# Performance work log

Measured on AMD Instinct MI355X. Metric: run time of the kernel, lower is better.

Reference implementation:

```python
import jax, jax.numpy as jnp
import numpy as np

N = 50000        # nodes
E = 800000       # edges (before self-loops)
F_IN = 128       # in_features
HID = 128        # hidden_size
HEADS = 4
NEG_SLOPE = 0.2  # PyG GATConv default


def setup_inputs() -> dict:
    key = jax.random.key(0)
    ks = jax.random.split(key, 16)
    def w(k, shape, fan_in):
        return jax.random.normal(k, shape, dtype=jnp.float32) / np.sqrt(fan_in)
    x = jax.random.normal(ks[0], (N, F_IN), dtype=jnp.float32)
    edge_index = jax.random.randint(ks[1], (2, E), 0, N, dtype=jnp.int64)
    return {
        "x": x,
        "edge_index": edge_index,
        # encoder: HEADS independent GATConv(F_IN -> HID, heads=1)
        "enc_W": w(ks[2], (HEADS, F_IN, HID), F_IN),
        "enc_asrc": w(ks[3], (HEADS, HID), HID),
        "enc_adst": w(ks[4], (HEADS, HID), HID),
        "enc_b": jnp.zeros((HEADS, HID), jnp.float32),
        "enc_lin_W": w(ks[5], (HEADS * HID, HID), HEADS * HID),
        "enc_lin_b": jnp.zeros((HID,), jnp.float32),
        # decoder: HEADS independent GATConv(HID -> F_IN, heads=1)
        "dec_W": w(ks[6], (HEADS, HID, F_IN), HID),
        "dec_asrc": w(ks[7], (HEADS, F_IN), F_IN),
        "dec_adst": w(ks[8], (HEADS, F_IN), F_IN),
        "dec_b": jnp.zeros((HEADS, F_IN), jnp.float32),
        "dec_lin_W": w(ks[9], (HEADS * F_IN, F_IN), HEADS * F_IN),
        "dec_lin_b": jnp.zeros((F_IN,), jnp.float32),
    }


def _gat_head(x, src, dst, W, a_src, a_dst, b, n):
    # PyG GATConv, heads=1: h = xW; e = leaky_relu(a_src.h_src + a_dst.h_dst)
    # alpha = segment-softmax over incoming edges of dst; out = scatter-add + b
    h = x @ W                                   # [n, out]
    e = (h @ a_src)[src] + (h @ a_dst)[dst]     # [Etot]
    e = jax.nn.leaky_relu(e, NEG_SLOPE)
    m = jax.ops.segment_max(e, dst, num_segments=n)
    ew = jnp.exp(e - m[dst])
    denom = jax.ops.segment_sum(ew, dst, num_segments=n)
    alpha = ew / denom[dst]                     # self-loops guarantee denom > 0
    out = jax.ops.segment_sum(alpha[:, None] * h[src], dst, num_segments=n)
    return out + b


def _multihead(x, src, dst, Ws, asrc, adst, bs, lin_W, lin_b, n):
    heads = [_gat_head(x, src, dst, Ws[h], asrc[h], adst[h], bs[h], n)
             for h in range(Ws.shape[0])]
    cat = jnp.concatenate(heads, axis=1)        # [n, heads*out]
    return jax.nn.relu(cat @ lin_W + lin_b)


def reference(x, edge_index, enc_W, enc_asrc, enc_adst, enc_b, enc_lin_W,
              enc_lin_b, dec_W, dec_asrc, dec_adst, dec_b, dec_lin_W,
              dec_lin_b):
    n = x.shape[0]
    loop = jnp.arange(n, dtype=edge_index.dtype)
    src = jnp.concatenate([edge_index[0], loop])  # add self-loops (PyG default)
    dst = jnp.concatenate([edge_index[1], loop])
    enc = _multihead(x, src, dst, enc_W, enc_asrc, enc_adst, enc_b,
                     enc_lin_W, enc_lin_b, n)
    dec = _multihead(enc, src, dst, dec_W, dec_asrc, dec_adst, dec_b,
                     dec_lin_W, dec_lin_b, n)
    return dec
```

## Files before the change

kernel.cpp:

```cpp
#include <hip/hip_runtime.h>
#include <hip/hip_fp16.h>
#include <cstdint>
#include <cstddef>


#define FDIM   128
#define HEADS  4
#define HCAT   512

typedef unsigned short u16;
typedef __attribute__((ext_vector_type(4))) float f32x4;
typedef __attribute__((ext_vector_type(8))) _Float16 f16x8;

__device__ __forceinline__ u16 f2h_bits(float f) {
    _Float16 h = (_Float16)f;
    return *(u16*)&h;
}

__global__ void k_detect_zero(const void* ei, int E, int N, int* flag, int* deg) {
    int i = blockIdx.x * blockDim.x + threadIdx.x;
    if (i < N) deg[i] = 0;
    if (i == 0) {
        const long long* p = (const long long*)ei;
        int bad = 0;
        int n = E < 64 ? E : 64;
        for (int k = 0; k < n; ++k) {
            long long v = p[k];
            if (v < 0 || v >= (long long)N) bad = 1;
        }
        *flag = bad;
    }
}

__device__ __forceinline__ int edge_at(const void* ei, int is32, long long pos) {
    return is32 ? ((const int*)ei)[pos] : (int)(((const long long*)ei)[pos]);
}

__global__ void k_count(const void* ei, const int* flag, int E, int N, int* deg) {
    int e = blockIdx.x * blockDim.x + threadIdx.x;
    int Etot = E + N;
    if (e >= Etot) return;
    int is32 = *flag;
    int dst = (e < E) ? edge_at(ei, is32, (long long)E + e) : (e - E);
    atomicAdd(&deg[dst], 1);
}

#define SCAN_BLOCKS 256
#define SCAN_TPB    256

__global__ __launch_bounds__(SCAN_TPB) void k_scan1(const int* __restrict__ deg,
                                                    int* __restrict__ bsum, int N) {
    __shared__ int sdata[SCAN_TPB];
    int b = blockIdx.x;
    int chunk = (N + SCAN_BLOCKS - 1) / SCAN_BLOCKS;
    int start = b * chunk;
    int end = start + chunk;
    if (start > N) start = N;
    if (end > N) end = N;
    int s = 0;
    for (int i = start + threadIdx.x; i < end; i += SCAN_TPB) s += deg[i];
    sdata[threadIdx.x] = s;
    __syncthreads();
    for (int o = SCAN_TPB / 2; o; o >>= 1) {
        if (threadIdx.x < o) sdata[threadIdx.x] += sdata[threadIdx.x + o];
        __syncthreads();
    }
    if (threadIdx.x == 0) bsum[b] = sdata[0];
}

__global__ __launch_bounds__(SCAN_BLOCKS) void k_scan2(const int* __restrict__ bsum,
                                                       int* __restrict__ bbase,
                                                       int* __restrict__ off_last) {
    __shared__ int sdata[SCAN_BLOCKS];
    int t = threadIdx.x;
    sdata[t] = bsum[t];
    __syncthreads();
    for (int o = 1; o < SCAN_BLOCKS; o <<= 1) {
        int v = (t >= o) ? sdata[t - o] : 0;
        __syncthreads();
        sdata[t] += v;
        __syncthreads();
    }
    bbase[t] = (t == 0) ? 0 : sdata[t - 1];
    if (t == SCAN_BLOCKS - 1) *off_last = sdata[t];
}

__global__ __launch_bounds__(SCAN_TPB) void k_scan3(const int* __restrict__ deg,
                                                    const int* __restrict__ bbase,
                                                    int* __restrict__ off,
                                                    int* __restrict__ cur, int N) {
    __shared__ int sdata[SCAN_TPB];
    int b = blockIdx.x;
    int chunk = (N + SCAN_BLOCKS - 1) / SCAN_BLOCKS;
    int start = b * chunk;
    int end = start + chunk;
    if (start > N) start = N;
    if (end > N) end = N;
    int base = bbase[b];
    for (int i0 = start; i0 < end; i0 += SCAN_TPB) {
        int i = i0 + threadIdx.x;
        int v = (i < end) ? deg[i] : 0;
        sdata[threadIdx.x] = v;
        __syncthreads();
        for (int o = 1; o < SCAN_TPB; o <<= 1) {
            int u = (threadIdx.x >= o) ? sdata[threadIdx.x - o] : 0;
            __syncthreads();
            sdata[threadIdx.x] += u;
            __syncthreads();
        }
        if (i < end) {
            int excl = base + sdata[threadIdx.x] - v;
            off[i] = excl;
            cur[i] = excl;
        }
        base += sdata[SCAN_TPB - 1];
        __syncthreads();
    }
}

__global__ void k_fill(const void* ei, const int* flag, int E, int N, int* cur, int* csr) {
    int e = blockIdx.x * blockDim.x + threadIdx.x;
    int Etot = E + N;
    if (e >= Etot) return;
    int is32 = *flag;
    int src, dst;
    if (e < E) {
        src = edge_at(ei, is32, e);
        dst = edge_at(ei, is32, (long long)E + e);
    } else {
        src = e - E;
        dst = e - E;
    }
    int pos = atomicAdd(&cur[dst], 1);
    csr[pos] = src;
}

__global__ void k_prep(const float* __restrict__ x, u16* __restrict__ xh, int Nf,
                       const float* __restrict__ encW, u16* __restrict__ eh,
                       const float* __restrict__ linW, u16* __restrict__ lh,
                       const float* __restrict__ decW, u16* __restrict__ dh,
                       const float* __restrict__ dlW, u16* __restrict__ dh2) {
    int i = blockIdx.x * blockDim.x + threadIdx.x;
    if (i < Nf) {
        xh[i] = f2h_bits(x[i]);
        return;
    }
    int j = i - Nf;
    const int WSZ = HEADS * FDIM * FDIM;
    const float* W;
    u16* hi;
    int K;
    if (j < WSZ)            { W = encW; hi = eh;  K = FDIM; }
    else if (j < 2 * WSZ)   { W = linW; hi = lh;  K = HCAT; j -= WSZ; }
    else if (j < 3 * WSZ)   { W = decW; hi = dh;  K = FDIM; j -= 2 * WSZ; }
    else if (j < 4 * WSZ)   { W = dlW;  hi = dh2; K = HCAT; j -= 3 * WSZ; }
    else return;
    int blk = j / (K * 128);
    int rem = j - blk * K * 128;
    int k = rem >> 7, col = rem & 127;
    hi[(size_t)blk * 128 * K + (size_t)col * K + k] = f2h_bits(W[j]);
}

template <int MODE>
__global__ __launch_bounds__(256) void k_gemm_f16(
    const u16* __restrict__ A, int lda,
    const u16* __restrict__ Bt,
    const float* __restrict__ bias,
    const float* __restrict__ asrc, const float* __restrict__ adst,
    float* __restrict__ C, u16* __restrict__ Cb1,
    float* __restrict__ ssrc, float* __restrict__ sdst,
    int ldc, int M, int K)
{
    __shared__ alignas(16) char smem[16384];
    __shared__ float sred[512];
    const int ASH = 0, BHI = 8192;
    int tid = threadIdx.x;
    int bm0 = blockIdx.x * 128;
    int yb = blockIdx.y;

    int wid = tid >> 6, lane = tid & 63;
    int wr = wid >> 1, wc = wid & 1;
    int fr = lane & 15, g = lane >> 4;

    f32x4 acc[4][4] = {};

    int arow = tid >> 1, ahalf = tid & 1;
    bool ain = (bm0 + arow) < M;
    const u16* aptr = A + (size_t)(bm0 + arow) * lda + ahalf * 16;
    int bcol = tid & 127, bhalf = tid >> 7;
    const u16* bph = Bt + (size_t)yb * 128 * K + (size_t)bcol * K + bhalf * 16;

    int abase = arow * 64 + ahalf * 32;
    int asw = (arow & 7) << 4;
    int bbase = bcol * 64 + bhalf * 32;
    int bsw = (bcol & 7) << 4;

    uint4 va0, va1, vb0, vb1;
    if (ain) { va0 = *(const uint4*)(aptr); va1 = *(const uint4*)(aptr + 8); }
    else { va0 = make_uint4(0, 0, 0, 0); va1 = make_uint4(0, 0, 0, 0); }
    vb0 = *(const uint4*)(bph);
    vb1 = *(const uint4*)(bph + 8);

    for (int k0 = 0; k0 < K; k0 += 32) {
        *(uint4*)(smem + ASH + ((abase +  0) ^ asw)) = va0;
        *(uint4*)(smem + ASH + ((abase + 16) ^ asw)) = va1;
        *(uint4*)(smem + BHI + ((bbase +  0) ^ bsw)) = vb0;
        *(uint4*)(smem + BHI + ((bbase + 16) ^ bsw)) = vb1;

        __syncthreads();

        if (k0 + 32 < K) {
            int kn = k0 + 32;
            if (ain) { va0 = *(const uint4*)(aptr + kn); va1 = *(const uint4*)(aptr + kn + 8); }
            else { va0 = make_uint4(0, 0, 0, 0); va1 = make_uint4(0, 0, 0, 0); }
            vb0 = *(const uint4*)(bph + kn);
            vb1 = *(const uint4*)(bph + kn + 8);
        }

        f16x8 af[4], bh[4];
#pragma unroll
        for (int mi = 0; mi < 4; ++mi) {
            int r = wr * 64 + mi * 16 + fr;
            int off = (r * 64 + g * 16) ^ ((r & 7) << 4);
            af[mi] = *(f16x8*)(smem + ASH + off);
        }
#pragma unroll
        for (int nj = 0; nj < 4; ++nj) {
            int c = wc * 64 + nj * 16 + fr;
            int off = (c * 64 + g * 16) ^ ((c & 7) << 4);
            bh[nj] = *(f16x8*)(smem + BHI + off);
        }

#pragma unroll
        for (int mi = 0; mi < 4; ++mi)
#pragma unroll
            for (int nj = 0; nj < 4; ++nj)
                acc[mi][nj] = __builtin_amdgcn_mfma_f32_16x16x32_f16(af[mi], bh[nj], acc[mi][nj], 0, 0, 0);
        __syncthreads();
    }

#pragma unroll
    for (int mi = 0; mi < 4; ++mi) {
#pragma unroll
        for (int q = 0; q < 4; ++q) {
            int r = bm0 + wr * 64 + mi * 16 + g * 4 + q;
            if (r >= M) continue;
#pragma unroll
            for (int nj = 0; nj < 4; ++nj) {
                int c = wc * 64 + nj * 16 + fr;
                float v = acc[mi][nj][q];
                if (MODE == 0) {
                    Cb1[(size_t)r * ldc + yb * 128 + c] = f2h_bits(v);
                } else if (MODE == 1) {
                    v += bias[c];
                    v = fmaxf(v, 0.f);
                    Cb1[(size_t)r * ldc + c] = f2h_bits(v);
                } else {
                    v += bias[c];
                    v = fmaxf(v, 0.f);
                    C[(size_t)r * ldc + c] = v;
                }
            }
        }
    }

    if (MODE == 0) {
        float asv[4], adv[4];
        const float* app = asrc + yb * FDIM;
        const float* dpp = adst + yb * FDIM;
#pragma unroll
        for (int nj = 0; nj < 4; ++nj) {
            int c = wc * 64 + nj * 16 + fr;
            asv[nj] = app[c];
            adv[nj] = dpp[c];
        }
#pragma unroll
        for (int mi = 0; mi < 4; ++mi) {
#pragma unroll
            for (int q = 0; q < 4; ++q) {
                float ps = 0.f, pd = 0.f;
#pragma unroll
                for (int nj = 0; nj < 4; ++nj) {
                    ps += acc[mi][nj][q] * asv[nj];
                    pd += acc[mi][nj][q] * adv[nj];
                }
#pragma unroll
                for (int o = 1; o < 16; o <<= 1) {
                    ps += __shfl_xor(ps, o);
                    pd += __shfl_xor(pd, o);
                }
                if (fr == 0) {
                    int row128 = wr * 64 + mi * 16 + g * 4 + q;
                    sred[(row128 * 2 + wc) * 2 + 0] = ps;
                    sred[(row128 * 2 + wc) * 2 + 1] = pd;
                }
            }
        }
        __syncthreads();
        {
            int rg = tid >> 1;
            int which = tid & 1;
            int r = bm0 + rg;
            if (r < M) {
                float v = sred[(rg * 2 + 0) * 2 + which] + sred[(rg * 2 + 1) * 2 + which];
                float* dstp = which ? sdst : ssrc;
                dstp[(size_t)yb * M + r] = v;
            }
        }
    }
}

__global__ __launch_bounds__(64) void k_aggregate(
    const u16* __restrict__ Hb, const int* __restrict__ off,
    const int* __restrict__ csr, const float* __restrict__ ssrc,
    const float* __restrict__ sdst, const float* __restrict__ bvec,
    u16* __restrict__ Gh, int N) {
    int n = blockIdx.x;
    int lane = threadIdx.x;
    int o0 = __builtin_amdgcn_readfirstlane(off[n]);
    int o1 = __builtin_amdgcn_readfirstlane(off[n + 1]);
    int h = lane >> 4;
    int col0 = lane * 8;
    float sdh = sdst[(size_t)h * N + n];
    const float* ssrc_h = ssrc + (size_t)h * N;
    float denom = 0.f;
    float acc[8] = {0.f, 0.f, 0.f, 0.f, 0.f, 0.f, 0.f, 0.f};

    auto body = [&](float ew, uint4 hv) {
        const __half2* hp = (const __half2*)&hv;
#pragma unroll
        for (int j = 0; j < 4; ++j) {
            float2 f = __half22float2(hp[j]);
            acc[2 * j]     += ew * f.x;
            acc[2 * j + 1] += ew * f.y;
        }
    };

    int i = o0;
    for (; i + 4 <= o1; i += 4) {
        int s0 = csr[i + 0], s1 = csr[i + 1], s2 = csr[i + 2], s3 = csr[i + 3];
        uint4 v0 = *(const uint4*)&Hb[(size_t)s0 * HCAT + col0];
        uint4 v1 = *(const uint4*)&Hb[(size_t)s1 * HCAT + col0];
        uint4 v2 = *(const uint4*)&Hb[(size_t)s2 * HCAT + col0];
        uint4 v3 = *(const uint4*)&Hb[(size_t)s3 * HCAT + col0];
        float e0 = ssrc_h[s0] + sdh, e1 = ssrc_h[s1] + sdh;
        float e2 = ssrc_h[s2] + sdh, e3 = ssrc_h[s3] + sdh;
        e0 = e0 >= 0.f ? e0 : 0.2f * e0;
        e1 = e1 >= 0.f ? e1 : 0.2f * e1;
        e2 = e2 >= 0.f ? e2 : 0.2f * e2;
        e3 = e3 >= 0.f ? e3 : 0.2f * e3;
        float w0 = __expf(e0), w1 = __expf(e1), w2 = __expf(e2), w3 = __expf(e3);
        denom += (w0 + w1) + (w2 + w3);
        body(w0, v0);
        body(w1, v1);
        body(w2, v2);
        body(w3, v3);
    }
    for (; i < o1; ++i) {
        int s = csr[i];
        uint4 v = *(const uint4*)&Hb[(size_t)s * HCAT + col0];
        float e = ssrc_h[s] + sdh;
        e = e >= 0.f ? e : 0.2f * e;
        float ew = __expf(e);
        denom += ew;
        body(ew, v);
    }

    float inv = 1.f / denom;
    u16 hs[8];
#pragma unroll
    for (int k = 0; k < 8; ++k) {
        int col = col0 + k;
        float v = acc[k] * inv + bvec[h * FDIM + (col & 127)];
        hs[k] = f2h_bits(v);
    }
    *(uint4*)&Gh[(size_t)n * HCAT + col0] = *(uint4*)hs;
}

extern "C" void kernel_launch(void* const* d_in, const int* in_sizes, int n_in,
                              void* d_out, int out_size, void* d_ws, size_t ws_size,
                              hipStream_t stream) {
    const float* x = (const float*)d_in[0];
    const void* ei = d_in[1];
    const float* encW = (const float*)d_in[2];
    const float* enc_asrc = (const float*)d_in[3];
    const float* enc_adst = (const float*)d_in[4];
    const float* enc_b = (const float*)d_in[5];
    const float* enc_linW = (const float*)d_in[6];
    const float* enc_linb = (const float*)d_in[7];
    const float* decW = (const float*)d_in[8];
    const float* dec_asrc = (const float*)d_in[9];
    const float* dec_adst = (const float*)d_in[10];
    const float* dec_b = (const float*)d_in[11];
    const float* dec_linW = (const float*)d_in[12];
    const float* dec_linb = (const float*)d_in[13];

    int N = in_sizes[0] / FDIM;
    int E = in_sizes[1] / 2;
    int Etot = E + N;

    char* w = (char*)d_ws;
    size_t o = 0;
    auto alloc = [&](size_t bytes) -> char* {
        char* p = w + o;
        o += (bytes + 255) & ~(size_t)255;
        return p;
    };
    int* flag = (int*)alloc(4);
    int* deg = (int*)alloc((size_t)N * 4);
    int* off = (int*)alloc((size_t)(N + 1) * 4);
    int* cur = (int*)alloc((size_t)N * 4);
    int* csr = (int*)alloc((size_t)Etot * 4);
    int* bsum = (int*)alloc(SCAN_BLOCKS * 4);
    int* bbase = (int*)alloc(SCAN_BLOCKS * 4);
    float* ssrc = (float*)alloc((size_t)HEADS * N * 4);
    float* sdst = (float*)alloc((size_t)HEADS * N * 4);
    u16* Gh = (u16*)alloc((size_t)N * HCAT * 2);
    u16* Hb = (u16*)alloc((size_t)N * HCAT * 2);
    u16* xh = (u16*)alloc((size_t)N * FDIM * 2);
    u16* X2h = (u16*)alloc((size_t)N * FDIM * 2);
    u16* encWt_h = (u16*)alloc((size_t)HEADS * FDIM * FDIM * 2);
    u16* linWt_h = (u16*)alloc((size_t)HCAT * FDIM * 2);
    u16* decWt_h = (u16*)alloc((size_t)HEADS * FDIM * FDIM * 2);
    u16* dlinWt_h = (u16*)alloc((size_t)HCAT * FDIM * 2);
    (void)ws_size;

    k_detect_zero<<<(N + 255) / 256, 256, 0, stream>>>(ei, E, N, flag, deg);
    k_count<<<(Etot + 255) / 256, 256, 0, stream>>>(ei, flag, E, N, deg);
    k_scan1<<<SCAN_BLOCKS, SCAN_TPB, 0, stream>>>(deg, bsum, N);
    k_scan2<<<1, SCAN_BLOCKS, 0, stream>>>(bsum, bbase, off + N);
    k_scan3<<<SCAN_BLOCKS, SCAN_TPB, 0, stream>>>(deg, bbase, off, cur, N);
    k_fill<<<(Etot + 255) / 256, 256, 0, stream>>>(ei, flag, E, N, cur, csr);

    int Nf = N * FDIM;
    int prep_total = Nf + 4 * HEADS * FDIM * FDIM;
    k_prep<<<(prep_total + 255) / 256, 256, 0, stream>>>(
        x, xh, Nf,
        encW, encWt_h,
        enc_linW, linWt_h,
        decW, decWt_h,
        dec_linW, dlinWt_h);

    int mblocks = (N + 127) / 128;

    k_gemm_f16<0><<<dim3(mblocks, 4), 256, 0, stream>>>(
        xh, FDIM, encWt_h, nullptr, enc_asrc, enc_adst,
        nullptr, Hb, ssrc, sdst, HCAT, N, FDIM);
    k_aggregate<<<N, 64, 0, stream>>>(Hb, off, csr, ssrc, sdst, enc_b, Gh, N);
    k_gemm_f16<1><<<dim3(mblocks, 1), 256, 0, stream>>>(
        Gh, HCAT, linWt_h, enc_linb, nullptr, nullptr,
        nullptr, X2h, nullptr, nullptr, FDIM, N, HCAT);

    k_gemm_f16<0><<<dim3(mblocks, 4), 256, 0, stream>>>(
        X2h, FDIM, decWt_h, nullptr, dec_asrc, dec_adst,
        nullptr, Hb, ssrc, sdst, HCAT, N, FDIM);
    k_aggregate<<<N, 64, 0, stream>>>(Hb, off, csr, ssrc, sdst, dec_b, Gh, N);
    k_gemm_f16<2><<<dim3(mblocks, 1), 256, 0, stream>>>(
        Gh, HCAT, dlinWt_h, dec_linb, nullptr, nullptr,
        (float*)d_out, nullptr, nullptr, nullptr, FDIM, N, HCAT);
}
```

Measured before the change: 491.1 us.

## Load full K=128 tiles once in head GEMM and pack four nodes per aggregate block

Adds a dedicated head-projection GEMM that loads the whole 128-deep A and B tiles into 64KB of LDS in one pass, removing the per-k-step double sync loop. The linear GEMMs keep the pipelined loop but drop the head-score epilogue. The aggregate kernel now runs four nodes per 256-thread block instead of one node per 64-thread block, cutting the block count and per-block launch overhead. The larger LDS use may lower GEMM occupancy.

```diff
diff --git a/kernel.cpp b/kernel.cpp
--- a/kernel.cpp
+++ b/kernel.cpp
@@ -161,19 +161,17 @@
     hi[(size_t)blk * 128 * K + (size_t)col * K + k] = f2h_bits(W[j]);
 }
 
-template <int MODE>
-__global__ __launch_bounds__(256) void k_gemm_f16(
-    const u16* __restrict__ A, int lda,
+__global__ __launch_bounds__(256) void k_headgemm(
+    const u16* __restrict__ A,
     const u16* __restrict__ Bt,
-    const float* __restrict__ bias,
     const float* __restrict__ asrc, const float* __restrict__ adst,
-    float* __restrict__ C, u16* __restrict__ Cb1,
+    u16* __restrict__ Hb,
     float* __restrict__ ssrc, float* __restrict__ sdst,
-    int ldc, int M, int K)
+    int M)
 {
-    __shared__ alignas(16) char smem[16384];
+    __shared__ alignas(16) char smem[65536];
     __shared__ float sred[512];
-    const int ASH = 0, BHI = 8192;
+    const int ASH = 0, BSH = 32768;
     int tid = threadIdx.x;
     int bm0 = blockIdx.x * 128;
     int yb = blockIdx.y;
@@ -182,61 +180,42 @@
     int wr = wid >> 1, wc = wid & 1;
     int fr = lane & 15, g = lane >> 4;
 
+    {
+        int row = tid >> 1, half = tid & 1;
+        bool ain = (bm0 + row) < M;
+        const u16* ap = A + (size_t)(bm0 + row) * FDIM + half * 64;
+        const u16* bp = Bt + ((size_t)yb * 128 + row) * FDIM + half * 64;
+        int sw = (row & 7) << 4;
+#pragma unroll
+        for (int j = 0; j < 8; ++j) {
+            uint4 va = ain ? *(const uint4*)(ap + j * 8) : make_uint4(0, 0, 0, 0);
+            uint4 vb = *(const uint4*)(bp + j * 8);
+            *(uint4*)(smem + ASH + ((row * 256 + half * 128 + j * 16) ^ sw)) = va;
+            *(uint4*)(smem + BSH + ((row * 256 + half * 128 + j * 16) ^ sw)) = vb;
+        }
+    }
+    __syncthreads();
+
     f32x4 acc[4][4] = {};
-
-    int arow = tid >> 1, ahalf = tid & 1;
-    bool ain = (bm0 + arow) < M;
-    const u16* aptr = A + (size_t)(bm0 + arow) * lda + ahalf * 16;
-    int bcol = tid & 127, bhalf = tid >> 7;
-    const u16* bph = Bt + (size_t)yb * 128 * K + (size_t)bcol * K + bhalf * 16;
-
-    int abase = arow * 64 + ahalf * 32;
-    int asw = (arow & 7) << 4;
-    int bbase = bcol * 64 + bhalf * 32;
-    int bsw = (bcol & 7) << 4;
-
-    uint4 va0, va1, vb0, vb1;
-    if (ain) { va0 = *(const uint4*)(aptr); va1 = *(const uint4*)(aptr + 8); }
-    else { va0 = make_uint4(0, 0, 0, 0); va1 = make_uint4(0, 0, 0, 0); }
-    vb0 = *(const uint4*)(bph);
-    vb1 = *(const uint4*)(bph + 8);
-
-    for (int k0 = 0; k0 < K; k0 += 32) {
-        *(uint4*)(smem + ASH + ((abase +  0) ^ asw)) = va0;
-        *(uint4*)(smem + ASH + ((abase + 16) ^ asw)) = va1;
-        *(uint4*)(smem + BHI + ((bbase +  0) ^ bsw)) = vb0;
-        *(uint4*)(smem + BHI + ((bbase + 16) ^ bsw)) = vb1;
-
-        __syncthreads();
-
-        if (k0 + 32 < K) {
-            int kn = k0 + 32;
-            if (ain) { va0 = *(const uint4*)(aptr + kn); va1 = *(const uint4*)(aptr + kn + 8); }
-            else { va0 = make_uint4(0, 0, 0, 0); va1 = make_uint4(0, 0, 0, 0); }
-            vb0 = *(const uint4*)(bph + kn);
-            vb1 = *(const uint4*)(bph + kn + 8);
-        }
-
+#pragma unroll
+    for (int ks = 0; ks < 4; ++ks) {
+        int kb = ks * 64 + g * 16;
         f16x8 af[4], bh[4];
 #pragma unroll
         for (int mi = 0; mi < 4; ++mi) {
             int r = wr * 64 + mi * 16 + fr;
-            int off = (r * 64 + g * 16) ^ ((r & 7) << 4);
-            af[mi] = *(f16x8*)(smem + ASH + off);
+            af[mi] = *(f16x8*)(smem + ASH + ((r * 256 + kb) ^ ((r & 7) << 4)));
         }
 #pragma unroll
         for (int nj = 0; nj < 4; ++nj) {
             int c = wc * 64 + nj * 16 + fr;
-            int off = (c * 64 + g * 16) ^ ((c & 7) << 4);
-            bh[nj] = *(f16x8*)(smem + BHI + off);
-        }
-
+            bh[nj] = *(f16x8*)(smem + BSH + ((c * 256 + kb) ^ ((c & 7) << 4)));
+        }
 #pragma unroll
         for (int mi = 0; mi < 4; ++mi)
 #pragma unroll
             for (int nj = 0; nj < 4; ++nj)
                 acc[mi][nj] = __builtin_amdgcn_mfma_f32_16x16x32_f16(af[mi], bh[nj], acc[mi][nj], 0, 0, 0);
-        __syncthreads();
     }
 
 #pragma unroll
@@ -248,23 +227,12 @@
 #pragma unroll
             for (int nj = 0; nj < 4; ++nj) {
                 int c = wc * 64 + nj * 16 + fr;
-                float v = acc[mi][nj][q];
-                if (MODE == 0) {
-                    Cb1[(size_t)r * ldc + yb * 128 + c] = f2h_bits(v);
-                } else if (MODE == 1) {
-                    v += bias[c];
-                    v = fmaxf(v, 0.f);
-                    Cb1[(size_t)r * ldc + c] = f2h_bits(v);
-                } else {
-                    v += bias[c];
-                    v = fmaxf(v, 0.f);
-                    C[(size_t)r * ldc + c] = v;
-                }
+                Hb[(size_t)r * HCAT + yb * 128 + c] = f2h_bits(acc[mi][nj][q]);
             }
         }
     }
 
-    if (MODE == 0) {
+    {
         float asv[4], adv[4];
         const float* app = asrc + yb * FDIM;
         const float* dpp = adst + yb * FDIM;
@@ -310,13 +278,110 @@
     }
 }
 
-__global__ __launch_bounds__(64) void k_aggregate(
+template <int MODE>
+__global__ __launch_bounds__(256) void k_gemm_f16(
+    const u16* __restrict__ A, int lda,
+    const u16* __restrict__ Bt,
+    const float* __restrict__ bias,
+    float* __restrict__ C, u16* __restrict__ Cb1,
+    int ldc, int M, int K)
+{
+    __shared__ alignas(16) char smem[16384];
+    const int ASH = 0, BHI = 8192;
+    int tid = threadIdx.x;
+    int bm0 = blockIdx.x * 128;
+
+    int wid = tid >> 6, lane = tid & 63;
+    int wr = wid >> 1, wc = wid & 1;
+    int fr = lane & 15, g = lane >> 4;
+
+    f32x4 acc[4][4] = {};
+
+    int arow = tid >> 1, ahalf = tid & 1;
+    bool ain = (bm0 + arow) < M;
+    const u16* aptr = A + (size_t)(bm0 + arow) * lda + ahalf * 16;
+    int bcol = tid & 127, bhalf = tid >> 7;
+    const u16* bph = Bt + (size_t)bcol * K + bhalf * 16;
+
+    int abase = arow * 64 + ahalf * 32;
+    int asw = (arow & 7) << 4;
+    int bbase = bcol * 64 + bhalf * 32;
+    int bsw = (bcol & 7) << 4;
+
+    uint4 va0, va1, vb0, vb1;
+    if (ain) { va0 = *(const uint4*)(aptr); va1 = *(const uint4*)(aptr + 8); }
+    else { va0 = make_uint4(0, 0, 0, 0); va1 = make_uint4(0, 0, 0, 0); }
+    vb0 = *(const uint4*)(bph);
+    vb1 = *(const uint4*)(bph + 8);
+
+    for (int k0 = 0; k0 < K; k0 += 32) {
+        *(uint4*)(smem + ASH + ((abase +  0) ^ asw)) = va0;
+        *(uint4*)(smem + ASH + ((abase + 16) ^ asw)) = va1;
+        *(uint4*)(smem + BHI + ((bbase +  0) ^ bsw)) = vb0;
+        *(uint4*)(smem + BHI + ((bbase + 16) ^ bsw)) = vb1;
+
+        __syncthreads();
+
+        if (k0 + 32 < K) {
+            int kn = k0 + 32;
+            if (ain) { va0 = *(const uint4*)(aptr + kn); va1 = *(const uint4*)(aptr + kn + 8); }
+            else { va0 = make_uint4(0, 0, 0, 0); va1 = make_uint4(0, 0, 0, 0); }
+            vb0 = *(const uint4*)(bph + kn);
+            vb1 = *(const uint4*)(bph + kn + 8);
+        }
+
+        f16x8 af[4], bh[4];
+#pragma unroll
+        for (int mi = 0; mi < 4; ++mi) {
+            int r = wr * 64 + mi * 16 + fr;
+            int off = (r * 64 + g * 16) ^ ((r & 7) << 4);
+            af[mi] = *(f16x8*)(smem + ASH + off);
+        }
+#pragma unroll
+        for (int nj = 0; nj < 4; ++nj) {
+            int c = wc * 64 + nj * 16 + fr;
+            int off = (c * 64 + g * 16) ^ ((c & 7) << 4);
+            bh[nj] = *(f16x8*)(smem + BHI + off);
+        }
+
+#pragma unroll
+        for (int mi = 0; mi < 4; ++mi)
+#pragma unroll
+            for (int nj = 0; nj < 4; ++nj)
+                acc[mi][nj] = __builtin_amdgcn_mfma_f32_16x16x32_f16(af[mi], bh[nj], acc[mi][nj], 0, 0, 0);
+        __syncthreads();
+    }
+
+#pragma unroll
+    for (int mi = 0; mi < 4; ++mi) {
+#pragma unroll
+        for (int q = 0; q < 4; ++q) {
+            int r = bm0 + wr * 64 + mi * 16 + g * 4 + q;
+            if (r >= M) continue;
+#pragma unroll
+            for (int nj = 0; nj < 4; ++nj) {
+                int c = wc * 64 + nj * 16 + fr;
+                float v = acc[mi][nj][q];
+                v += bias[c];
+                v = fmaxf(v, 0.f);
+                if (MODE == 1) {
+                    Cb1[(size_t)r * ldc + c] = f2h_bits(v);
+                } else {
+                    C[(size_t)r * ldc + c] = v;
+                }
+            }
+        }
+    }
+}
+
+__global__ __launch_bounds__(256) void k_aggregate(
     const u16* __restrict__ Hb, const int* __restrict__ off,
     const int* __restrict__ csr, const float* __restrict__ ssrc,
     const float* __restrict__ sdst, const float* __restrict__ bvec,
     u16* __restrict__ Gh, int N) {
-    int n = blockIdx.x;
-    int lane = threadIdx.x;
+    int n = blockIdx.x * 4 + (threadIdx.x >> 6);
+    if (n >= N) return;
+    int lane = threadIdx.x & 63;
     int o0 = __builtin_amdgcn_readfirstlane(off[n]);
     int o1 = __builtin_amdgcn_readfirstlane(off[n + 1]);
     int h = lane >> 4;
@@ -442,20 +507,17 @@
         dec_linW, dlinWt_h);
 
     int mblocks = (N + 127) / 128;
-
-    k_gemm_f16<0><<<dim3(mblocks, 4), 256, 0, stream>>>(
-        xh, FDIM, encWt_h, nullptr, enc_asrc, enc_adst,
-        nullptr, Hb, ssrc, sdst, HCAT, N, FDIM);
-    k_aggregate<<<N, 64, 0, stream>>>(Hb, off, csr, ssrc, sdst, enc_b, Gh, N);
+    int aggblocks = (N + 3) / 4;
+
+    k_headgemm<<<dim3(mblocks, 4), 256, 0, stream>>>(
+        xh, encWt_h, enc_asrc, enc_adst, Hb, ssrc, sdst, N);
+    k_aggregate<<<aggblocks, 256, 0, stream>>>(Hb, off, csr, ssrc, sdst, enc_b, Gh, N);
     k_gemm_f16<1><<<dim3(mblocks, 1), 256, 0, stream>>>(
-        Gh, HCAT, linWt_h, enc_linb, nullptr, nullptr,
-        nullptr, X2h, nullptr, nullptr, FDIM, N, HCAT);
-
-    k_gemm_f16<0><<<dim3(mblocks, 4), 256, 0, stream>>>(
-        X2h, FDIM, decWt_h, nullptr, dec_asrc, dec_adst,
-        nullptr, Hb, ssrc, sdst, HCAT, N, FDIM);
-    k_aggregate<<<N, 64, 0, stream>>>(Hb, off, csr, ssrc, sdst, dec_b, Gh, N);
+        Gh, HCAT, linWt_h, enc_linb, nullptr, X2h, FDIM, N, HCAT);
+
+    k_headgemm<<<dim3(mblocks, 4), 256, 0, stream>>>(
+        X2h, decWt_h, dec_asrc, dec_adst, Hb, ssrc, sdst, N);
+    k_aggregate<<<aggblocks, 256, 0, stream>>>(Hb, off, csr, ssrc, sdst, dec_b, Gh, N);
     k_gemm_f16<2><<<dim3(mblocks, 1), 256, 0, stream>>>(
-        Gh, HCAT, dlinWt_h, dec_linb, nullptr, nullptr,
-        (float*)d_out, nullptr, nullptr, nullptr, FDIM, N, HCAT);
-}
+        Gh, HCAT, dlinWt_h, dec_linb, (float*)d_out, nullptr, FDIM, N, HCAT);
+}
```

Measured after the change: 498.4 us. About the same (+1.5%).
